# Optimization experiments

Hardware: AMD Instinct MI355X
Metric: run time of the kernel (lower is better)

## Reference

```python
import jax, jax.numpy as jnp
import numpy as np

N_NODES = 50000
N_GRAPHS = 512
HIDDEN = 128
BN_EPS = 1e-5


def setup_inputs() -> dict:
    key = jax.random.key(0)
    ks = jax.random.split(key, 16)
    E = 800000
    x = jax.random.normal(ks[0], (N_NODES, 1), dtype=jnp.float32)
    pos = jax.random.normal(ks[1], (N_NODES, 3), dtype=jnp.float32)
    edge_index = jax.random.randint(ks[2], (2, E), 0, N_NODES, dtype=jnp.int64)
    batch = jnp.sort(jax.random.randint(ks[3], (N_NODES,), 0, N_GRAPHS, dtype=jnp.int64))

    def lin(k, fan_in, fan_out):
        bound = 1.0 / np.sqrt(fan_in)
        return jax.random.uniform(k, (fan_in, fan_out), jnp.float32, -bound, bound)

    # conv1: in=1 -> concat dim 2*1+3=5
    c1_w1 = lin(ks[4], 5, HIDDEN); c1_b1 = jnp.zeros((HIDDEN,), jnp.float32)
    c1_w2 = lin(ks[5], HIDDEN, HIDDEN); c1_b2 = jnp.zeros((HIDDEN,), jnp.float32)
    # conv2: in=128 -> concat dim 2*128+3=259
    c2_w1 = lin(ks[6], 2 * HIDDEN + 3, HIDDEN); c2_b1 = jnp.zeros((HIDDEN,), jnp.float32)
    c2_w2 = lin(ks[7], HIDDEN, HIDDEN); c2_b2 = jnp.zeros((HIDDEN,), jnp.float32)
    # predictor MLP [128, 128, 1], bias=[False, True], batch_norm + relu between
    p_w1 = lin(ks[8], HIDDEN, HIDDEN)
    bn_gamma = jnp.ones((HIDDEN,), jnp.float32)
    bn_beta = jnp.zeros((HIDDEN,), jnp.float32)
    p_w2 = lin(ks[9], HIDDEN, 1)
    p_b2 = jnp.zeros((1,), jnp.float32)
    return {
        "x": x, "pos": pos, "edge_index": edge_index, "batch": batch,
        "c1_w1": c1_w1, "c1_b1": c1_b1, "c1_w2": c1_w2, "c1_b2": c1_b2,
        "c2_w1": c2_w1, "c2_b1": c2_b1, "c2_w2": c2_w2, "c2_b2": c2_b2,
        "p_w1": p_w1, "bn_gamma": bn_gamma, "bn_beta": bn_beta,
        "p_w2": p_w2, "p_b2": p_b2,
    }


def _conv(x, pos, src, dst, w1, b1, w2, b2):
    # gather endpoints; PyG: x_j = x[src], x_i = x[dst], aggregate into dst
    feat = jnp.concatenate([x[dst], x[src], pos[src] - pos[dst]], axis=-1)  # [E, 2F+3]
    msg = jax.nn.relu(feat @ w1 + b1) @ w2 + b2  # [E, H]
    return jax.ops.segment_sum(msg, dst, num_segments=N_NODES)  # [N, H]


def reference(x, pos, edge_index, batch,
              c1_w1, c1_b1, c1_w2, c1_b2,
              c2_w1, c2_b1, c2_w2, c2_b2,
              p_w1, bn_gamma, bn_beta, p_w2, p_b2):
    src, dst = edge_index[0], edge_index[1]
    h = jax.nn.relu(_conv(x, pos, src, dst, c1_w1, c1_b1, c1_w2, c1_b2))
    h = jax.nn.relu(_conv(h, pos, src, dst, c2_w1, c2_b1, c2_w2, c2_b2))
    g = jax.ops.segment_sum(h, batch, num_segments=N_GRAPHS)  # [G, H] global add pool
    # predictor: Linear(no bias) -> BatchNorm(train stats) -> ReLU -> Linear(bias)
    z = g @ p_w1
    mean = jnp.mean(z, axis=0)
    var = jnp.var(z, axis=0)
    z = bn_gamma * (z - mean) * jax.lax.rsqrt(var + BN_EPS) + bn_beta
    z = jax.nn.relu(z)
    return z @ p_w2 + p_b2  # [G, 1]
```

## Files before the change

### kernel.cpp

```cpp
#include <hip/hip_runtime.h>
#include <hip/hip_bf16.h>

#define HID 128
#define DMAX 64
#define ESHARD 2048

typedef unsigned int uint;
typedef unsigned short ushort;
using short8 = __attribute__((ext_vector_type(8))) short;
using f32x4  = __attribute__((ext_vector_type(4))) float;

#define MFMA_B16(a, b, c) __builtin_amdgcn_mfma_f32_16x16x32_bf16(a, b, c, 0, 0, 0)

__device__ inline ushort bf16rn(float f) {
  uint u = __float_as_uint(f);
  u += 0x7fff + ((u >> 16) & 1);
  return (ushort)(u >> 16);
}
__device__ inline uint packbf(float a, float b) {
  return (uint)bf16rn(a) | ((uint)bf16rn(b) << 16);
}
__device__ inline float bflo(uint u) { return __uint_as_float(u << 16); }
__device__ inline float bfhi(uint u) { return __uint_as_float(u & 0xffff0000u); }

__global__ __launch_bounds__(256) void k_prep(
    const float* __restrict__ x, const float* __restrict__ pos,
    const float* __restrict__ c1w2, const float* __restrict__ c2w1, const float* __restrict__ c2w2,
    float4* __restrict__ xp, int* __restrict__ deg, float* __restrict__ g,
    float* __restrict__ mv,
    ushort* __restrict__ w1t, ushort* __restrict__ wdt,
    ushort* __restrict__ wst, ushort* __restrict__ w2t,
    int N, int G, int Npad) {
  int idx = blockIdx.x * 256 + threadIdx.x;
  if (idx < Npad) deg[idx] = 0;
  if (idx < G * HID) g[idx] = 0.f;
  if (idx < 256) mv[idx] = 0.f;
  if (idx < N) {
    xp[idx] = make_float4(pos[3 * idx], pos[3 * idx + 1], pos[3 * idx + 2], x[idx]);
  }
  {
    int m = idx >> 14, e = idx & 16383;
    int c = e >> 7, k = e & 127;
    const float* src;
    ushort* dst;
    if (m == 0)      { src = c1w2;              dst = w1t; }
    else if (m == 1) { src = c2w1;              dst = wdt; }
    else if (m == 2) { src = c2w1 + 128 * 128;  dst = wst; }
    else             { src = c2w2;              dst = w2t; }
    dst[e] = bf16rn(src[k * 128 + c]);
  }
}

__global__ __launch_bounds__(256) void k_build(const int* __restrict__ dstv,
                                               const int* __restrict__ srcv,
                                               int* __restrict__ deg, int* __restrict__ srcsP,
                                               int E) {
  int shard = blockIdx.x & 7;
  int base = (blockIdx.x >> 3) * ESHARD;
  int lim = min(base + ESHARD, E);
  for (int e = base + threadIdx.x; e < lim; e += 256) {
    int d = dstv[e];
    if (((d >> 5) & 7) == shard) {
      int s = srcv[e];
      int r = atomicAdd(&deg[d], 1);
      if (r < DMAX) srcsP[(size_t)d * DMAX + r] = s;
    }
  }
}

__global__ __launch_bounds__(64) void k_conv1(
    const float4* __restrict__ xp,
    const int* __restrict__ deg, const int* __restrict__ srcsP,
    const float* __restrict__ w1, const float* __restrict__ b1, uint* __restrict__ hs) {
  int n = blockIdx.x;
  int lane = threadIdx.x;
  int f0 = 2 * lane;
  __shared__ float sxs[64];
  __shared__ float sdp[3][64];
  int cnt = min(deg[n], DMAX);
  float4 me = xp[n];
  float xi = me.w;
  float2 a1 = *(const float2*)&w1[HID + f0];
  float2 a2 = *(const float2*)&w1[2 * HID + f0];
  float2 a3 = *(const float2*)&w1[3 * HID + f0];
  float2 a4 = *(const float2*)&w1[4 * HID + f0];
  float c_0 = fmaf(xi, w1[f0],     b1[f0]);
  float c_1 = fmaf(xi, w1[f0 + 1], b1[f0 + 1]);
  float acc0 = 0.f, acc1 = 0.f;
  if (lane < cnt) {
    int s = srcsP[(size_t)n * DMAX + lane];
    float4 v = xp[s];
    sxs[lane] = v.w;
    sdp[0][lane] = v.x - me.x;
    sdp[1][lane] = v.y - me.y;
    sdp[2][lane] = v.z - me.z;
  }
  __syncthreads();
  for (int k = 0; k < cnt; ++k) {
    float xj = sxs[k], d0 = sdp[0][k], d1 = sdp[1][k], d2 = sdp[2][k];
    float h0 = fmaf(xj, a1.x, fmaf(d0, a2.x, fmaf(d1, a3.x, fmaf(d2, a4.x, c_0))));
    float h1 = fmaf(xj, a1.y, fmaf(d0, a2.y, fmaf(d1, a3.y, fmaf(d2, a4.y, c_1))));
    acc0 += fmaxf(h0, 0.f);
    acc1 += fmaxf(h1, 0.f);
  }
  hs[(size_t)n * 64 + lane] = packbf(acc0, acc1);
}

__global__ __launch_bounds__(512) void k_mfuse(
    const ushort* __restrict__ A, const ushort* __restrict__ W1t,
    const ushort* __restrict__ Wdt, const ushort* __restrict__ Wst,
    const float* __restrict__ b1, const float* __restrict__ bd,
    const int* __restrict__ deg,
    uint* __restrict__ psb, uint* __restrict__ pdb, int M) {
  __shared__ uint hl[64][68];
  __shared__ uint hd[64][68];
  int t = threadIdx.x;
  int l = t & 63;
  int rl = l & 15, kg = l >> 4;
  int wv = t >> 6;
  int rg = wv & 3;
  int cg = wv >> 2;
  int rloc = rg * 16 + rl;
  int r = blockIdx.x * 64 + rloc;
  int rc = min(r, M - 1);
  bool valid = (r < M);
  const short8* arow = (const short8*)(A + (size_t)rc * 128);
  short8 af0 = arow[kg], af1 = arow[4 + kg], af2 = arow[8 + kg], af3 = arow[12 + kg];
  float dg = valid ? (float)deg[r] : 0.f;
  #pragma unroll
  for (int ntl = 0; ntl < 4; ++ntl) {
    int nt = cg * 4 + ntl;
    const short8* wrow = (const short8*)(W1t + (size_t)(nt * 16 + rl) * 128);
    f32x4 acc = {0.f, 0.f, 0.f, 0.f};
    acc = MFMA_B16(wrow[kg],      af0, acc);
    acc = MFMA_B16(wrow[4 + kg],  af1, acc);
    acc = MFMA_B16(wrow[8 + kg],  af2, acc);
    acc = MFMA_B16(wrow[12 + kg], af3, acc);
    int c0 = nt * 16 + kg * 4;
    f32x4 b4 = *(const f32x4*)&b1[c0];
    float v0 = fmaxf(fmaf(dg, b4[0], acc[0]), 0.f);
    float v1 = fmaxf(fmaf(dg, b4[1], acc[1]), 0.f);
    float v2 = fmaxf(fmaf(dg, b4[2], acc[2]), 0.f);
    float v3 = fmaxf(fmaf(dg, b4[3], acc[3]), 0.f);
    hl[rloc][(c0 >> 1)]     = packbf(v0, v1);
    hl[rloc][(c0 >> 1) + 1] = packbf(v2, v3);
  }
  __syncthreads();
  const uint* hrow = hl[rloc];
  short8 bfrag[4];
  #pragma unroll
  for (int i = 0; i < 4; ++i) bfrag[i] = *(const short8*)&hrow[i * 16 + kg * 4];
  __syncthreads();
  #pragma unroll
  for (int ntl = 0; ntl < 4; ++ntl) {
    int nt = cg * 4 + ntl;
    const short8* wsrow = (const short8*)(Wst + (size_t)(nt * 16 + rl) * 128);
    const short8* wdrow = (const short8*)(Wdt + (size_t)(nt * 16 + rl) * 128);
    f32x4 accS = {0.f, 0.f, 0.f, 0.f};
    f32x4 accD = {0.f, 0.f, 0.f, 0.f};
    accS = MFMA_B16(wsrow[kg],      bfrag[0], accS);
    accS = MFMA_B16(wsrow[4 + kg],  bfrag[1], accS);
    accS = MFMA_B16(wsrow[8 + kg],  bfrag[2], accS);
    accS = MFMA_B16(wsrow[12 + kg], bfrag[3], accS);
    accD = MFMA_B16(wdrow[kg],      bfrag[0], accD);
    accD = MFMA_B16(wdrow[4 + kg],  bfrag[1], accD);
    accD = MFMA_B16(wdrow[8 + kg],  bfrag[2], accD);
    accD = MFMA_B16(wdrow[12 + kg], bfrag[3], accD);
    int c0 = nt * 16 + kg * 4;
    f32x4 b4 = *(const f32x4*)&bd[c0];
    hl[rloc][(c0 >> 1)]     = packbf(accS[0], accS[1]);
    hl[rloc][(c0 >> 1) + 1] = packbf(accS[2], accS[3]);
    hd[rloc][(c0 >> 1)]     = packbf(accD[0] + b4[0], accD[1] + b4[1]);
    hd[rloc][(c0 >> 1) + 1] = packbf(accD[2] + b4[2], accD[3] + b4[3]);
  }
  __syncthreads();
  int rbase = blockIdx.x * 64;
  #pragma unroll
  for (int idx = t; idx < 64 * 16; idx += 512) {
    int row = idx >> 4, c4 = (idx & 15) * 4;
    int gr = rbase + row;
    if (gr < M) {
      *(uint4*)&psb[(size_t)gr * 64 + c4] = *(const uint4*)&hl[row][c4];
      *(uint4*)&pdb[(size_t)gr * 64 + c4] = *(const uint4*)&hd[row][c4];
    }
  }
}

__global__ __launch_bounds__(64) void k_conv2(
    const float4* __restrict__ xp,
    const int* __restrict__ deg, const int* __restrict__ srcsP,
    const uint* __restrict__ pdb, const uint* __restrict__ ps,
    const float* __restrict__ wc, uint* __restrict__ hs) {
  int n = blockIdx.x;
  int lane = threadIdx.x;
  int eg = lane >> 4;
  int fb = lane & 15;
  int f0 = 8 * fb;
  __shared__ int ssrc[64];
  __shared__ float sdp[3][64];
  int cnt = min(deg[n], DMAX);
  float4 me = xp[n];
  float c0[8], c1[8], c2[8], pdv[8], acc[8];
  uint4 pdu = *(const uint4*)&pdb[(size_t)n * 64 + fb * 4];
  uint pdua[4] = {pdu.x, pdu.y, pdu.z, pdu.w};
  #pragma unroll
  for (int i = 0; i < 4; ++i) {
    pdv[2 * i]     = bflo(pdua[i]);
    pdv[2 * i + 1] = bfhi(pdua[i]);
  }
  #pragma unroll
  for (int i = 0; i < 8; ++i) {
    c0[i]  = wc[f0 + i];
    c1[i]  = wc[HID + f0 + i];
    c2[i]  = wc[2 * HID + f0 + i];
    acc[i] = 0.f;
  }
  if (lane < cnt) {
    int s = srcsP[(size_t)n * DMAX + lane];
    float4 v = xp[s];
    ssrc[lane] = s;
    sdp[0][lane] = v.x - me.x;
    sdp[1][lane] = v.y - me.y;
    sdp[2][lane] = v.z - me.z;
  }
  __syncthreads();
  for (int k = 0; k < cnt; k += 16) {
    int ke[4] = {k + eg, k + 4 + eg, k + 8 + eg, k + 12 + eg};
    int kc[4];
    #pragma unroll
    for (int j = 0; j < 4; ++j) kc[j] = min(ke[j], cnt - 1);
    int se[4] = {ssrc[kc[0]], ssrc[kc[1]], ssrc[kc[2]], ssrc[kc[3]]};
    uint4 u[4];
    #pragma unroll
    for (int j = 0; j < 4; ++j) u[j] = *(const uint4*)&ps[(size_t)se[j] * 64 + fb * 4];
    #pragma unroll
    for (int j = 0; j < 4; ++j) {
      float dd0 = sdp[0][kc[j]], dd1 = sdp[1][kc[j]], dd2 = sdp[2][kc[j]];
      bool vv = ke[j] < cnt;
      uint uu[4] = {u[j].x, u[j].y, u[j].z, u[j].w};
      if (vv) {
        #pragma unroll
        for (int q = 0; q < 4; ++q) {
          float w0  = pdv[2*q]   + fmaf(dd0, c0[2*q],   fmaf(dd1, c1[2*q],   dd2 * c2[2*q]));
          float w1v = pdv[2*q+1] + fmaf(dd0, c0[2*q+1], fmaf(dd1, c1[2*q+1], dd2 * c2[2*q+1]));
          acc[2*q]   += fmaxf(w0  + bflo(uu[q]), 0.f);
          acc[2*q+1] += fmaxf(w1v + bfhi(uu[q]), 0.f);
        }
      }
    }
  }
  #pragma unroll
  for (int i = 0; i < 8; ++i) {
    acc[i] += __shfl_xor(acc[i], 16);
    acc[i] += __shfl_xor(acc[i], 32);
  }
  if (eg == 0) {
    uint4 o;
    o.x = packbf(acc[0], acc[1]);
    o.y = packbf(acc[2], acc[3]);
    o.z = packbf(acc[4], acc[5]);
    o.w = packbf(acc[6], acc[7]);
    *(uint4*)&hs[(size_t)n * 64 + fb * 4] = o;
  }
}

__global__ __launch_bounds__(256) void k_mpool(
    const ushort* __restrict__ A, const ushort* __restrict__ Wt,
    const float* __restrict__ bias, const int* __restrict__ deg, const int* __restrict__ batch,
    float* __restrict__ Of, int M) {
  int t = threadIdx.x;
  int l = t & 63;
  int rl = l & 15, kg = l >> 4;
  int r = blockIdx.x * 64 + (t >> 6) * 16 + rl;
  int rc = min(r, M - 1);
  bool valid = (r < M);
  const short8* arow = (const short8*)(A + (size_t)rc * 128);
  short8 af0 = arow[kg], af1 = arow[4 + kg], af2 = arow[8 + kg], af3 = arow[12 + kg];
  float dg = valid ? (float)deg[r] : 0.f;
  int bt = batch[rc];
  int gf = __shfl(bt, 0);
  int gl = __shfl(bt, 15);
  #pragma unroll
  for (int nt = 0; nt < 8; ++nt) {
    const short8* wrow = (const short8*)(Wt + (size_t)(nt * 16 + rl) * 128);
    f32x4 acc = {0.f, 0.f, 0.f, 0.f};
    acc = MFMA_B16(wrow[kg],      af0, acc);
    acc = MFMA_B16(wrow[4 + kg],  af1, acc);
    acc = MFMA_B16(wrow[8 + kg],  af2, acc);
    acc = MFMA_B16(wrow[12 + kg], af3, acc);
    int c0 = nt * 16 + kg * 4;
    f32x4 b4 = *(const f32x4*)&bias[c0];
    float v0 = valid ? fmaxf(fmaf(dg, b4[0], acc[0]), 0.f) : 0.f;
    float v1 = valid ? fmaxf(fmaf(dg, b4[1], acc[1]), 0.f) : 0.f;
    float v2 = valid ? fmaxf(fmaf(dg, b4[2], acc[2]), 0.f) : 0.f;
    float v3 = valid ? fmaxf(fmaf(dg, b4[3], acc[3]), 0.f) : 0.f;
    for (int gg = gf; gg <= gl; ++gg) {
      bool mine = (bt == gg);
      float s0 = mine ? v0 : 0.f;
      float s1 = mine ? v1 : 0.f;
      float s2 = mine ? v2 : 0.f;
      float s3 = mine ? v3 : 0.f;
      #pragma unroll
      for (int m = 1; m <= 8; m <<= 1) {
        s0 += __shfl_xor(s0, m);
        s1 += __shfl_xor(s1, m);
        s2 += __shfl_xor(s2, m);
        s3 += __shfl_xor(s3, m);
      }
      if (rl == 0) {
        float* gp = &Of[(size_t)gg * 128 + c0];
        atomicAdd(gp + 0, s0);
        atomicAdd(gp + 1, s1);
        atomicAdd(gp + 2, s2);
        atomicAdd(gp + 3, s3);
      }
    }
  }
}

__global__ __launch_bounds__(256) void k_pgemm(
    const float* __restrict__ A, const float* __restrict__ W, float* __restrict__ O1,
    float* __restrict__ mv, int M) {
  __shared__ float As[128][36];
  int t = threadIdx.x;
  int n0 = blockIdx.x * 32;
  int j = t & 127, m = t >> 7;
  for (int idx = t; idx < 32 * 128; idx += 256) {
    int r = idx >> 7, i = idx & 127;
    int n = n0 + r;
    As[i][r] = (n < M) ? A[(size_t)n * 128 + i] : 0.f;
  }
  __syncthreads();
  float acc[16];
  #pragma unroll
  for (int r = 0; r < 16; ++r) acc[r] = 0.f;
  int rb = m * 16;
  for (int i = 0; i < 128; ++i) {
    float w = W[i * 128 + j];
    const float4* ap = reinterpret_cast<const float4*>(&As[i][rb]);
    #pragma unroll
    for (int q = 0; q < 4; ++q) {
      float4 a = ap[q];
      acc[q * 4 + 0] = fmaf(a.x, w, acc[q * 4 + 0]);
      acc[q * 4 + 1] = fmaf(a.y, w, acc[q * 4 + 1]);
      acc[q * 4 + 2] = fmaf(a.z, w, acc[q * 4 + 2]);
      acc[q * 4 + 3] = fmaf(a.w, w, acc[q * 4 + 3]);
    }
  }
  float S = 0.f, Q = 0.f;
  #pragma unroll
  for (int r = 0; r < 16; ++r) {
    int n = n0 + rb + r;
    if (n < M) {
      O1[(size_t)n * 128 + j] = acc[r];
      S += acc[r];
      Q = fmaf(acc[r], acc[r], Q);
    }
  }
  atomicAdd(&mv[j], S);
  atomicAdd(&mv[128 + j], Q);
}

__global__ __launch_bounds__(256) void k_final(
    const float* __restrict__ z, const float* __restrict__ mv,
    const float* __restrict__ gamma, const float* __restrict__ beta,
    const float* __restrict__ w2, const float* __restrict__ b2,
    float* __restrict__ out, int G) {
  int wid = threadIdx.x >> 6, lane = threadIdx.x & 63;
  int r = blockIdx.x * 4 + wid;
  if (r >= G) return;
  float acc = 0.f;
  float invG = 1.f / (float)G;
  #pragma unroll
  for (int h = 0; h < 2; ++h) {
    int jj = lane + h * 64;
    float mean = mv[jj] * invG;
    float var = mv[128 + jj] * invG - mean * mean;
    float rstd = rsqrtf(var + 1e-5f);
    float v = z[(size_t)r * 128 + jj];
    float zn = fmaf((v - mean) * rstd, gamma[jj], beta[jj]);
    acc = fmaf(fmaxf(zn, 0.f), w2[jj], acc);
  }
  #pragma unroll
  for (int off = 32; off; off >>= 1) acc += __shfl_down(acc, off);
  if (lane == 0) out[r] = acc + b2[0];
}

extern "C" void kernel_launch(void* const* d_in, const int* in_sizes, int n_in,
                              void* d_out, int out_size, void* d_ws, size_t ws_size,
                              hipStream_t stream) {
  const float* x     = (const float*)d_in[0];
  const float* pos   = (const float*)d_in[1];
  const int*   eidx  = (const int*)d_in[2];
  const int*   batch = (const int*)d_in[3];
  const float* c1w1  = (const float*)d_in[4];
  const float* c1b1  = (const float*)d_in[5];
  const float* c1w2  = (const float*)d_in[6];
  const float* c1b2  = (const float*)d_in[7];
  const float* c2w1  = (const float*)d_in[8];
  const float* c2b1  = (const float*)d_in[9];
  const float* c2w2  = (const float*)d_in[10];
  const float* c2b2  = (const float*)d_in[11];
  const float* pw1   = (const float*)d_in[12];
  const float* gamma = (const float*)d_in[13];
  const float* beta  = (const float*)d_in[14];
  const float* pw2   = (const float*)d_in[15];
  const float* pb2   = (const float*)d_in[16];
  (void)n_in; (void)ws_size;

  const int N = in_sizes[0];
  const int E = in_sizes[2] / 2;
  const int G = out_size;
  const int* srcv = eidx;
  const int* dstv = eidx + E;

  char* w = (char*)d_ws;
  size_t o = 0;
  auto carve = [&](size_t bytes) { void* p = w + o; o = (o + bytes + 255) & ~(size_t)255; return p; };
  int Npad = ((N + 255) / 256) * 256;
  int* deg    = (int*)carve((size_t)Npad * 4);
  int* srcsP  = (int*)carve((size_t)N * DMAX * 4);
  float4* xp  = (float4*)carve((size_t)N * 16);
  uint*   hs1  = (uint*)carve((size_t)N * 64 * 4);
  uint*   pdb  = (uint*)carve((size_t)N * 64 * 4);
  uint*   psb  = (uint*)carve((size_t)N * 64 * 4);
  uint*   hs2  = (uint*)carve((size_t)N * 64 * 4);
  ushort* w1t  = (ushort*)carve(16384 * 2);
  ushort* wdt  = (ushort*)carve(16384 * 2);
  ushort* wst  = (ushort*)carve(16384 * 2);
  ushort* w2t  = (ushort*)carve(16384 * 2);
  float* g    = (float*)carve((size_t)G * HID * 4);
  float* z    = (float*)carve((size_t)G * HID * 4);
  float* mv   = (float*)carve(256 * 4);

  k_prep<<<256, 256, 0, stream>>>(x, pos, c1w2, c2w1, c2w2,
                                  xp, deg, g, mv, w1t, wdt, wst, w2t, N, G, Npad);
  int nwin = (E + ESHARD - 1) / ESHARD;
  k_build<<<nwin * 8, 256, 0, stream>>>(dstv, srcv, deg, srcsP, E);

  int gb = (N + 63) / 64;
  k_conv1<<<N, 64, 0, stream>>>(xp, deg, srcsP, c1w1, c1b1, hs1);
  k_mfuse<<<gb, 512, 0, stream>>>((const ushort*)hs1, w1t, wdt, wst, c1b2, c2b1, deg,
                                  psb, pdb, N);
  k_conv2<<<N, 64, 0, stream>>>(xp, deg, srcsP, pdb, psb, c2w1 + 256 * HID, hs2);
  k_mpool<<<gb, 256, 0, stream>>>((const ushort*)hs2, w2t, c2b2, deg, batch, g, N);
  k_pgemm<<<(G + 31) / 32, 256, 0, stream>>>(g, pw1, z, mv, G);
  k_final<<<(G + 3) / 4, 256, 0, stream>>>(z, mv, gamma, beta, pw2, pb2, (float*)d_out, G);
}
```

Before: 193.9 us.

## Fuse conv1 edge aggregation into the MFMA transform kernel

Merges the per-node conv1 aggregation kernel into the following MFMA kernel. Each of 8 waves aggregates 8 nodes into shared memory, and the GEMMs then read those rows directly instead of a global bf16 intermediate. This removes one launch and the write and read of the hs1 buffer. In exchange it adds 16 block-wide barriers inside the aggregation loop, and the per-node degree imbalance now stalls the whole 512-thread block.

Result: slower. 200.9 us (+3.6%).

```diff
diff --git a/kernel.cpp b/kernel.cpp
--- a/kernel.cpp
+++ b/kernel.cpp
@@ -68,52 +68,17 @@
   }
 }
 
-__global__ __launch_bounds__(64) void k_conv1(
+__global__ __launch_bounds__(512) void k_front(
     const float4* __restrict__ xp,
     const int* __restrict__ deg, const int* __restrict__ srcsP,
-    const float* __restrict__ w1, const float* __restrict__ b1, uint* __restrict__ hs) {
-  int n = blockIdx.x;
-  int lane = threadIdx.x;
-  int f0 = 2 * lane;
-  __shared__ float sxs[64];
-  __shared__ float sdp[3][64];
-  int cnt = min(deg[n], DMAX);
-  float4 me = xp[n];
-  float xi = me.w;
-  float2 a1 = *(const float2*)&w1[HID + f0];
-  float2 a2 = *(const float2*)&w1[2 * HID + f0];
-  float2 a3 = *(const float2*)&w1[3 * HID + f0];
-  float2 a4 = *(const float2*)&w1[4 * HID + f0];
-  float c_0 = fmaf(xi, w1[f0],     b1[f0]);
-  float c_1 = fmaf(xi, w1[f0 + 1], b1[f0 + 1]);
-  float acc0 = 0.f, acc1 = 0.f;
-  if (lane < cnt) {
-    int s = srcsP[(size_t)n * DMAX + lane];
-    float4 v = xp[s];
-    sxs[lane] = v.w;
-    sdp[0][lane] = v.x - me.x;
-    sdp[1][lane] = v.y - me.y;
-    sdp[2][lane] = v.z - me.z;
-  }
-  __syncthreads();
-  for (int k = 0; k < cnt; ++k) {
-    float xj = sxs[k], d0 = sdp[0][k], d1 = sdp[1][k], d2 = sdp[2][k];
-    float h0 = fmaf(xj, a1.x, fmaf(d0, a2.x, fmaf(d1, a3.x, fmaf(d2, a4.x, c_0))));
-    float h1 = fmaf(xj, a1.y, fmaf(d0, a2.y, fmaf(d1, a3.y, fmaf(d2, a4.y, c_1))));
-    acc0 += fmaxf(h0, 0.f);
-    acc1 += fmaxf(h1, 0.f);
-  }
-  hs[(size_t)n * 64 + lane] = packbf(acc0, acc1);
-}
-
-__global__ __launch_bounds__(512) void k_mfuse(
-    const ushort* __restrict__ A, const ushort* __restrict__ W1t,
-    const ushort* __restrict__ Wdt, const ushort* __restrict__ Wst,
+    const float* __restrict__ w1, const float* __restrict__ b1v,
+    const ushort* __restrict__ W1t, const ushort* __restrict__ Wdt, const ushort* __restrict__ Wst,
     const float* __restrict__ b1, const float* __restrict__ bd,
-    const int* __restrict__ deg,
     uint* __restrict__ psb, uint* __restrict__ pdb, int M) {
   __shared__ uint hl[64][68];
   __shared__ uint hd[64][68];
+  __shared__ float sxsw[8][64];
+  __shared__ float sdpw[8][3][64];
   int t = threadIdx.x;
   int l = t & 63;
   int rl = l & 15, kg = l >> 4;
@@ -122,20 +87,62 @@
   int cg = wv >> 2;
   int rloc = rg * 16 + rl;
   int r = blockIdx.x * 64 + rloc;
-  int rc = min(r, M - 1);
   bool valid = (r < M);
-  const short8* arow = (const short8*)(A + (size_t)rc * 128);
-  short8 af0 = arow[kg], af1 = arow[4 + kg], af2 = arow[8 + kg], af3 = arow[12 + kg];
   float dg = valid ? (float)deg[r] : 0.f;
+
+  int f0 = 2 * l;
+  float2 a1 = *(const float2*)&w1[HID + f0];
+  float2 a2 = *(const float2*)&w1[2 * HID + f0];
+  float2 a3 = *(const float2*)&w1[3 * HID + f0];
+  float2 a4 = *(const float2*)&w1[4 * HID + f0];
+  float w10 = w1[f0], w11 = w1[f0 + 1];
+  float b10 = b1v[f0], b11 = b1v[f0 + 1];
+  #pragma unroll
+  for (int q = 0; q < 8; ++q) {
+    int nloc = wv * 8 + q;
+    int n = blockIdx.x * 64 + nloc;
+    int nc = min(n, M - 1);
+    int cnt = (n < M) ? min(deg[n], DMAX) : 0;
+    float4 me = xp[nc];
+    if (l < cnt) {
+      int s = srcsP[(size_t)n * DMAX + l];
+      float4 v = xp[s];
+      sxsw[wv][l] = v.w;
+      sdpw[wv][0][l] = v.x - me.x;
+      sdpw[wv][1][l] = v.y - me.y;
+      sdpw[wv][2][l] = v.z - me.z;
+    }
+    __syncthreads();
+    float c_0 = fmaf(me.w, w10, b10);
+    float c_1 = fmaf(me.w, w11, b11);
+    float acc0 = 0.f, acc1 = 0.f;
+    for (int k = 0; k < cnt; ++k) {
+      float xj = sxsw[wv][k], d0 = sdpw[wv][0][k], d1 = sdpw[wv][1][k], d2 = sdpw[wv][2][k];
+      float h0 = fmaf(xj, a1.x, fmaf(d0, a2.x, fmaf(d1, a3.x, fmaf(d2, a4.x, c_0))));
+      float h1 = fmaf(xj, a1.y, fmaf(d0, a2.y, fmaf(d1, a3.y, fmaf(d2, a4.y, c_1))));
+      acc0 += fmaxf(h0, 0.f);
+      acc1 += fmaxf(h1, 0.f);
+    }
+    hl[nloc][l] = packbf(acc0, acc1);
+    __syncthreads();
+  }
+
+  short8 af[4];
+  {
+    const uint* hrow = hl[rloc];
+    #pragma unroll
+    for (int i = 0; i < 4; ++i) af[i] = *(const short8*)&hrow[i * 16 + kg * 4];
+  }
+  __syncthreads();
   #pragma unroll
   for (int ntl = 0; ntl < 4; ++ntl) {
     int nt = cg * 4 + ntl;
     const short8* wrow = (const short8*)(W1t + (size_t)(nt * 16 + rl) * 128);
     f32x4 acc = {0.f, 0.f, 0.f, 0.f};
-    acc = MFMA_B16(wrow[kg],      af0, acc);
-    acc = MFMA_B16(wrow[4 + kg],  af1, acc);
-    acc = MFMA_B16(wrow[8 + kg],  af2, acc);
-    acc = MFMA_B16(wrow[12 + kg], af3, acc);
+    acc = MFMA_B16(wrow[kg],      af[0], acc);
+    acc = MFMA_B16(wrow[4 + kg],  af[1], acc);
+    acc = MFMA_B16(wrow[8 + kg],  af[2], acc);
+    acc = MFMA_B16(wrow[12 + kg], af[3], acc);
     int c0 = nt * 16 + kg * 4;
     f32x4 b4 = *(const f32x4*)&b1[c0];
     float v0 = fmaxf(fmaf(dg, b4[0], acc[0]), 0.f);
@@ -146,10 +153,12 @@
     hl[rloc][(c0 >> 1) + 1] = packbf(v2, v3);
   }
   __syncthreads();
-  const uint* hrow = hl[rloc];
   short8 bfrag[4];
-  #pragma unroll
-  for (int i = 0; i < 4; ++i) bfrag[i] = *(const short8*)&hrow[i * 16 + kg * 4];
+  {
+    const uint* hrow = hl[rloc];
+    #pragma unroll
+    for (int i = 0; i < 4; ++i) bfrag[i] = *(const short8*)&hrow[i * 16 + kg * 4];
+  }
   __syncthreads();
   #pragma unroll
   for (int ntl = 0; ntl < 4; ++ntl) {
@@ -421,7 +430,6 @@
   int* deg    = (int*)carve((size_t)Npad * 4);
   int* srcsP  = (int*)carve((size_t)N * DMAX * 4);
   float4* xp  = (float4*)carve((size_t)N * 16);
-  uint*   hs1  = (uint*)carve((size_t)N * 64 * 4);
   uint*   pdb  = (uint*)carve((size_t)N * 64 * 4);
   uint*   psb  = (uint*)carve((size_t)N * 64 * 4);
   uint*   hs2  = (uint*)carve((size_t)N * 64 * 4);
@@ -439,9 +447,8 @@
   k_build<<<nwin * 8, 256, 0, stream>>>(dstv, srcv, deg, srcsP, E);
 
   int gb = (N + 63) / 64;
-  k_conv1<<<N, 64, 0, stream>>>(xp, deg, srcsP, c1w1, c1b1, hs1);
-  k_mfuse<<<gb, 512, 0, stream>>>((const ushort*)hs1, w1t, wdt, wst, c1b2, c2b1, deg,
-                                  psb, pdb, N);
+  k_front<<<gb, 512, 0, stream>>>(xp, deg, srcsP, c1w1, c1b1,
+                                  w1t, wdt, wst, c1b2, c2b1, psb, pdb, N);
   k_conv2<<<N, 64, 0, stream>>>(xp, deg, srcsP, pdb, psb, c2w1 + 256 * HID, hs2);
   k_mpool<<<gb, 256, 0, stream>>>((const ushort*)hs2, w2t, c2b2, deg, batch, g, N);
   k_pgemm<<<(G + 31) / 32, 256, 0, stream>>>(g, pw1, z, mv, G);
```

## Retile node-GEMM kernel to 128 rows per block with weight-fragment reuse

Applied to the files above, without the earlier changes.

The fused node-level GEMM kernel now handles 128 rows per block instead of 64. Each wave loads a weight fragment once and reuses it across four 16-row groups. The second stage gives each wave either the source or the destination projection. This cuts repeated global weight loads and halves the block count, at the cost of more registers, double the shared memory, and fewer blocks to spread across CUs.

Result: faster. 166.8 us, median of 2 (-14.0%).

```diff
diff --git a/kernel.cpp b/kernel.cpp
--- a/kernel.cpp
+++ b/kernel.cpp
@@ -112,73 +112,97 @@
     const float* __restrict__ b1, const float* __restrict__ bd,
     const int* __restrict__ deg,
     uint* __restrict__ psb, uint* __restrict__ pdb, int M) {
-  __shared__ uint hl[64][68];
-  __shared__ uint hd[64][68];
+  __shared__ uint hl[128][68];
+  __shared__ uint hd[128][68];
   int t = threadIdx.x;
   int l = t & 63;
   int rl = l & 15, kg = l >> 4;
   int wv = t >> 6;
-  int rg = wv & 3;
-  int cg = wv >> 2;
-  int rloc = rg * 16 + rl;
-  int r = blockIdx.x * 64 + rloc;
-  int rc = min(r, M - 1);
-  bool valid = (r < M);
-  const short8* arow = (const short8*)(A + (size_t)rc * 128);
-  short8 af0 = arow[kg], af1 = arow[4 + kg], af2 = arow[8 + kg], af3 = arow[12 + kg];
-  float dg = valid ? (float)deg[r] : 0.f;
-  #pragma unroll
-  for (int ntl = 0; ntl < 4; ++ntl) {
-    int nt = cg * 4 + ntl;
+  int rs = wv >> 2;
+  int ct = wv & 3;
+  int rowbase = blockIdx.x * 128 + rs * 64;
+  short8 af[4][4];
+  float dgv[4];
+  #pragma unroll
+  for (int rg = 0; rg < 4; ++rg) {
+    int r = rowbase + rg * 16 + rl;
+    int rc = min(r, M - 1);
+    const short8* arow = (const short8*)(A + (size_t)rc * 128);
+    #pragma unroll
+    for (int k = 0; k < 4; ++k) af[rg][k] = arow[4 * k + kg];
+    dgv[rg] = (r < M) ? (float)deg[r] : 0.f;
+  }
+  #pragma unroll
+  for (int j = 0; j < 2; ++j) {
+    int nt = ct * 2 + j;
     const short8* wrow = (const short8*)(W1t + (size_t)(nt * 16 + rl) * 128);
-    f32x4 acc = {0.f, 0.f, 0.f, 0.f};
-    acc = MFMA_B16(wrow[kg],      af0, acc);
-    acc = MFMA_B16(wrow[4 + kg],  af1, acc);
-    acc = MFMA_B16(wrow[8 + kg],  af2, acc);
-    acc = MFMA_B16(wrow[12 + kg], af3, acc);
+    short8 wf[4];
+    #pragma unroll
+    for (int k = 0; k < 4; ++k) wf[k] = wrow[4 * k + kg];
     int c0 = nt * 16 + kg * 4;
     f32x4 b4 = *(const f32x4*)&b1[c0];
-    float v0 = fmaxf(fmaf(dg, b4[0], acc[0]), 0.f);
-    float v1 = fmaxf(fmaf(dg, b4[1], acc[1]), 0.f);
-    float v2 = fmaxf(fmaf(dg, b4[2], acc[2]), 0.f);
-    float v3 = fmaxf(fmaf(dg, b4[3], acc[3]), 0.f);
-    hl[rloc][(c0 >> 1)]     = packbf(v0, v1);
-    hl[rloc][(c0 >> 1) + 1] = packbf(v2, v3);
-  }
-  __syncthreads();
-  const uint* hrow = hl[rloc];
-  short8 bfrag[4];
-  #pragma unroll
-  for (int i = 0; i < 4; ++i) bfrag[i] = *(const short8*)&hrow[i * 16 + kg * 4];
-  __syncthreads();
-  #pragma unroll
-  for (int ntl = 0; ntl < 4; ++ntl) {
-    int nt = cg * 4 + ntl;
-    const short8* wsrow = (const short8*)(Wst + (size_t)(nt * 16 + rl) * 128);
-    const short8* wdrow = (const short8*)(Wdt + (size_t)(nt * 16 + rl) * 128);
-    f32x4 accS = {0.f, 0.f, 0.f, 0.f};
-    f32x4 accD = {0.f, 0.f, 0.f, 0.f};
-    accS = MFMA_B16(wsrow[kg],      bfrag[0], accS);
-    accS = MFMA_B16(wsrow[4 + kg],  bfrag[1], accS);
-    accS = MFMA_B16(wsrow[8 + kg],  bfrag[2], accS);
-    accS = MFMA_B16(wsrow[12 + kg], bfrag[3], accS);
-    accD = MFMA_B16(wdrow[kg],      bfrag[0], accD);
-    accD = MFMA_B16(wdrow[4 + kg],  bfrag[1], accD);
-    accD = MFMA_B16(wdrow[8 + kg],  bfrag[2], accD);
-    accD = MFMA_B16(wdrow[12 + kg], bfrag[3], accD);
+    #pragma unroll
+    for (int rg = 0; rg < 4; ++rg) {
+      f32x4 acc = {0.f, 0.f, 0.f, 0.f};
+      acc = MFMA_B16(wf[0], af[rg][0], acc);
+      acc = MFMA_B16(wf[1], af[rg][1], acc);
+      acc = MFMA_B16(wf[2], af[rg][2], acc);
+      acc = MFMA_B16(wf[3], af[rg][3], acc);
+      int rloc = rs * 64 + rg * 16 + rl;
+      float v0 = fmaxf(fmaf(dgv[rg], b4[0], acc[0]), 0.f);
+      float v1 = fmaxf(fmaf(dgv[rg], b4[1], acc[1]), 0.f);
+      float v2 = fmaxf(fmaf(dgv[rg], b4[2], acc[2]), 0.f);
+      float v3 = fmaxf(fmaf(dgv[rg], b4[3], acc[3]), 0.f);
+      hl[rloc][(c0 >> 1)]     = packbf(v0, v1);
+      hl[rloc][(c0 >> 1) + 1] = packbf(v2, v3);
+    }
+  }
+  __syncthreads();
+  #pragma unroll
+  for (int rg = 0; rg < 4; ++rg) {
+    const uint* hrow = hl[rs * 64 + rg * 16 + rl];
+    #pragma unroll
+    for (int k = 0; k < 4; ++k) af[rg][k] = *(const short8*)&hrow[k * 16 + kg * 4];
+  }
+  __syncthreads();
+  bool isD = (ct >> 1) != 0;
+  int ntb = (ct & 1) * 4;
+  const ushort* Wm = isD ? Wdt : Wst;
+  #pragma unroll
+  for (int jj = 0; jj < 4; ++jj) {
+    int nt = ntb + jj;
+    const short8* wrow = (const short8*)(Wm + (size_t)(nt * 16 + rl) * 128);
+    short8 wf[4];
+    #pragma unroll
+    for (int k = 0; k < 4; ++k) wf[k] = wrow[4 * k + kg];
     int c0 = nt * 16 + kg * 4;
-    f32x4 b4 = *(const f32x4*)&bd[c0];
-    hl[rloc][(c0 >> 1)]     = packbf(accS[0], accS[1]);
-    hl[rloc][(c0 >> 1) + 1] = packbf(accS[2], accS[3]);
-    hd[rloc][(c0 >> 1)]     = packbf(accD[0] + b4[0], accD[1] + b4[1]);
-    hd[rloc][(c0 >> 1) + 1] = packbf(accD[2] + b4[2], accD[3] + b4[3]);
-  }
-  __syncthreads();
-  int rbase = blockIdx.x * 64;
-  #pragma unroll
-  for (int idx = t; idx < 64 * 16; idx += 512) {
+    f32x4 b4 = {0.f, 0.f, 0.f, 0.f};
+    if (isD) b4 = *(const f32x4*)&bd[c0];
+    #pragma unroll
+    for (int rg = 0; rg < 4; ++rg) {
+      f32x4 acc = {0.f, 0.f, 0.f, 0.f};
+      acc = MFMA_B16(wf[0], af[rg][0], acc);
+      acc = MFMA_B16(wf[1], af[rg][1], acc);
+      acc = MFMA_B16(wf[2], af[rg][2], acc);
+      acc = MFMA_B16(wf[3], af[rg][3], acc);
+      int rloc = rs * 64 + rg * 16 + rl;
+      uint lo = packbf(acc[0] + b4[0], acc[1] + b4[1]);
+      uint hi = packbf(acc[2] + b4[2], acc[3] + b4[3]);
+      if (isD) {
+        hd[rloc][(c0 >> 1)]     = lo;
+        hd[rloc][(c0 >> 1) + 1] = hi;
+      } else {
+        hl[rloc][(c0 >> 1)]     = lo;
+        hl[rloc][(c0 >> 1) + 1] = hi;
+      }
+    }
+  }
+  __syncthreads();
+  int rb2 = blockIdx.x * 128;
+  #pragma unroll
+  for (int idx = t; idx < 128 * 16; idx += 512) {
     int row = idx >> 4, c4 = (idx & 15) * 4;
-    int gr = rbase + row;
+    int gr = rb2 + row;
     if (gr < M) {
       *(uint4*)&psb[(size_t)gr * 64 + c4] = *(const uint4*)&hl[row][c4];
       *(uint4*)&pdb[(size_t)gr * 64 + c4] = *(const uint4*)&hd[row][c4];
@@ -438,11 +462,12 @@
   int nwin = (E + ESHARD - 1) / ESHARD;
   k_build<<<nwin * 8, 256, 0, stream>>>(dstv, srcv, deg, srcsP, E);
 
+  k_conv1<<<N, 64, 0, stream>>>(xp, deg, srcsP, c1w1, c1b1, hs1);
+  int gb128 = (N + 127) / 128;
+  k_mfuse<<<gb128, 512, 0, stream>>>((const ushort*)hs1, w1t, wdt, wst, c1b2, c2b1, deg,
+                                     psb, pdb, N);
+  k_conv2<<<N, 64, 0, stream>>>(xp, deg, srcsP, pdb, psb, c2w1 + 256 * HID, hs2);
   int gb = (N + 63) / 64;
-  k_conv1<<<N, 64, 0, stream>>>(xp, deg, srcsP, c1w1, c1b1, hs1);
-  k_mfuse<<<gb, 512, 0, stream>>>((const ushort*)hs1, w1t, wdt, wst, c1b2, c2b1, deg,
-                                  psb, pdb, N);
-  k_conv2<<<N, 64, 0, stream>>>(xp, deg, srcsP, pdb, psb, c2w1 + 256 * HID, hs2);
   k_mpool<<<gb, 256, 0, stream>>>((const ushort*)hs2, w2t, c2b2, deg, batch, g, N);
   k_pgemm<<<(G + 31) / 32, 256, 0, stream>>>(g, pw1, z, mv, G);
   k_final<<<(G + 3) / 4, 256, 0, stream>>>(z, mv, gamma, beta, pw2, pb2, (float*)d_out, G);
```
